# Optimization experiments

Hardware: AMD Instinct MI355X
Metric: run time of the kernel (lower is better)

The kernel has to match this reference:

```python
import jax, jax.numpy as jnp
from jax import lax
import numpy as np

B = 2; Hs = 48; Ws = 48
DIM = 768; NH = 6; NP = 4; DH = DIM // NH; HID = int(DIM * 0.25)
LIN = Hs * Ws                    # feat tokens (single deform level)
LQ = 21 * (Hs * Ws) // 4         # query tokens: (2H*2W)+(H*W)+(H/2*W/2)


def _ln(x, g, b, eps=1e-6):
    m = jnp.mean(x, -1, keepdims=True)
    v = jnp.mean((x - m) ** 2, -1, keepdims=True)
    return (x - m) * lax.rsqrt(v + eps) * g + b


def _bilinear_sample(value, loc, Hf, Wf):
    """value: [B,NH,Hf*Wf,DH]; loc: [B,Lq,NH,NP,2] normalized to [0,1].
    Matches F.grid_sample(align_corners=False, padding_mode='zeros')."""
    Bq, nH = value.shape[0], value.shape[1]
    Lq = loc.shape[1]
    x = loc[..., 0] * Wf - 0.5
    y = loc[..., 1] * Hf - 0.5
    x0 = jnp.floor(x); y0 = jnp.floor(y)
    wx1 = x - x0; wy1 = y - y0
    x0i = x0.astype(jnp.int32); y0i = y0.astype(jnp.int32)

    def tr(a):  # [B,Lq,NH,NP] -> [B,NH,Lq*NP]
        return jnp.transpose(a, (0, 2, 1, 3)).reshape(Bq, nH, Lq * NP)

    def gather(yi, xi):
        valid = ((xi >= 0) & (xi < Wf) & (yi >= 0) & (yi < Hf)).astype(value.dtype)
        idx = jnp.clip(yi, 0, Hf - 1) * Wf + jnp.clip(xi, 0, Wf - 1)
        g = jnp.take_along_axis(value, tr(idx)[..., None], axis=2)  # [B,NH,Lq*NP,DH]
        return g * tr(valid)[..., None]

    out = (gather(y0i, x0i) * tr((1 - wy1) * (1 - wx1))[..., None]
         + gather(y0i, x0i + 1) * tr((1 - wy1) * wx1)[..., None]
         + gather(y0i + 1, x0i) * tr(wy1 * (1 - wx1))[..., None]
         + gather(y0i + 1, x0i + 1) * tr(wy1 * wx1)[..., None])
    return out.reshape(Bq, nH, Lq, NP, DH)


def _dwconv(x_tokens, w, b, h, w_):
    Bq, n_tok, C = x_tokens.shape
    img = jnp.transpose(x_tokens, (0, 2, 1)).reshape(Bq, C, h, w_)
    y = lax.conv_general_dilated(img, w, (1, 1), 'SAME',
                                 dimension_numbers=('NCHW', 'OIHW', 'NCHW'),
                                 feature_group_count=C) + b[None, :, None, None]
    return jnp.transpose(y.reshape(Bq, C, h * w_), (0, 2, 1))


def _forward(query, reference_points, feat, qn_g, qn_b, fn_g, fn_b, vW, vb,
             soW, sob, awW, awb, opW, opb, mn_g, mn_b,
             fc1W, fc1b, dwW, dwb, fc2W, fc2b, H, W):
    Bq, Lq, C = query.shape
    q = _ln(query, qn_g, qn_b)
    v = _ln(feat, fn_g, fn_b) @ vW + vb                             # [B,Lin,C]
    value = jnp.transpose(v.reshape(Bq, -1, NH, DH), (0, 2, 1, 3))  # [B,NH,Lin,DH]
    offs = (q @ soW + sob).reshape(Bq, Lq, NH, NP, 2)
    attw = jax.nn.softmax((q @ awW + awb).reshape(Bq, Lq, NH, NP), axis=-1)
    norm = jnp.asarray([W, H], dtype=q.dtype)                       # (x,y) normalizer
    loc = reference_points.reshape(Bq, Lq, 1, 1, 2) + offs / norm   # [B,Lq,NH,NP,2]
    samp = _bilinear_sample(value, loc, H, W)                       # [B,NH,Lq,NP,DH]
    aw = jnp.transpose(attw, (0, 2, 1, 3))[..., None]               # [B,NH,Lq,NP,1]
    out = jnp.sum(samp * aw, axis=3)                                # [B,NH,Lq,DH]
    out = jnp.transpose(out, (0, 2, 1, 3)).reshape(Bq, Lq, C) @ opW + opb
    x = query + out                                                 # residual
    # multi-scale conv MLP
    h = _ln(x, mn_g, mn_b) @ fc1W + fc1b                            # [B,Lq,HID]
    n = Lq // 21
    h = jnp.concatenate([
        _dwconv(h[:, :16 * n], dwW, dwb, 2 * H, 2 * W),
        _dwconv(h[:, 16 * n:20 * n], dwW, dwb, H, W),
        _dwconv(h[:, 20 * n:], dwW, dwb, H // 2, W // 2)], axis=1)
    h = jax.nn.gelu(h, approximate=False)
    h = h @ fc2W + fc2b
    return x + h


def setup_inputs():
    key = jax.random.key(0)
    ks = jax.random.split(key, 16)
    s = 0.02
    return dict(
        query=jax.random.normal(ks[0], (B, LQ, DIM), jnp.float32),
        reference_points=jax.random.uniform(ks[1], (B, LQ, 1, 2), jnp.float32),
        feat=jax.random.normal(ks[2], (B, LIN, DIM), jnp.float32),
        spatial_shapes=jnp.array([[Hs, Ws]], jnp.int32),
        level_start_index=jnp.array([0], jnp.int32),
        H=Hs, W=Ws,
        qn_g=jnp.ones((DIM,)), qn_b=jnp.zeros((DIM,)),
        fn_g=jnp.ones((DIM,)), fn_b=jnp.zeros((DIM,)),
        mn_g=jnp.ones((DIM,)), mn_b=jnp.zeros((DIM,)),
        vW=s * jax.random.normal(ks[3], (DIM, DIM)), vb=jnp.zeros((DIM,)),
        soW=s * jax.random.normal(ks[4], (DIM, NH * NP * 2)),
        sob=0.5 * jax.random.normal(ks[5], (NH * NP * 2,)),
        awW=s * jax.random.normal(ks[6], (DIM, NH * NP)), awb=jnp.zeros((NH * NP,)),
        opW=s * jax.random.normal(ks[7], (DIM, DIM)), opb=jnp.zeros((DIM,)),
        fc1W=s * jax.random.normal(ks[8], (DIM, HID)), fc1b=jnp.zeros((HID,)),
        dwW=s * jax.random.normal(ks[9], (HID, 1, 3, 3)), dwb=jnp.zeros((HID,)),
        fc2W=s * jax.random.normal(ks[10], (HID, DIM)), fc2b=jnp.zeros((DIM,)),
    )


def reference(query, reference_points, feat, spatial_shapes, level_start_index, H, W,
              qn_g, qn_b, fn_g, fn_b, mn_g, mn_b, vW, vb, soW, sob, awW, awb,
              opW, opb, fc1W, fc1b, dwW, dwb, fc2W, fc2b):
    del spatial_shapes, level_start_index  # single level; H,W are static ints
    return _forward(query, reference_points, feat, qn_g, qn_b, fn_g, fn_b, vW, vb,
                    soW, sob, awW, awb, opW, opb, mn_g, mn_b,
                    fc1W, fc1b, dwW, dwb, fc2W, fc2b, H, W)
```

## Files before the change

kernel.cpp:

```cpp
#include <hip/hip_runtime.h>

#define NB    2
#define LQT   12096
#define LINT  2304
#define DIMC  768
#define NHD   6
#define NPT   4
#define DHD   128
#define HIDC  192
#define HH    48
#define WW    48

typedef __attribute__((ext_vector_type(8))) short bf16x8;
typedef __attribute__((ext_vector_type(4))) float f32x4;

__device__ __forceinline__ unsigned short f2bf(float f) {
  unsigned int u = __builtin_bit_cast(unsigned int, f);
  u += 0x7FFFu + ((u >> 16) & 1u);
  return (unsigned short)(u >> 16);
}
__device__ __forceinline__ float bf2f(unsigned short h) {
  unsigned int u = ((unsigned int)h) << 16;
  return __builtin_bit_cast(float, u);
}

__device__ __forceinline__ void gload16(const unsigned short* g, unsigned short* l) {
  __builtin_amdgcn_global_load_lds(
      (const __attribute__((address_space(1))) unsigned int*)g,
      (__attribute__((address_space(3))) unsigned int*)l, 16, 0, 0);
}

__global__ __launch_bounds__(256) void pack_wt(const float* __restrict__ src,
                                               unsigned short* __restrict__ dst,
                                               int K, int N, int rows) {
  size_t i = (size_t)blockIdx.x * 256 + threadIdx.x;
  if (i >= (size_t)rows * K) return;
  int n = (int)(i / K), k = (int)(i % K);
  float v = (n < N) ? src[(size_t)k * N + n] : 0.f;
  dst[i] = f2bf(v);
}

__global__ __launch_bounds__(256) void pack_soaw(const float* __restrict__ soW,
                                                 const float* __restrict__ awW,
                                                 const float* __restrict__ sob,
                                                 const float* __restrict__ awb,
                                                 unsigned short* __restrict__ dst,
                                                 float* __restrict__ bdst) {
  size_t i = (size_t)blockIdx.x * 256 + threadIdx.x;
  if (i < 128) bdst[i] = (i < 48) ? sob[i] : (i < 72 ? awb[i - 48] : 0.f);
  if (i >= (size_t)128 * DIMC) return;
  int n = (int)(i / DIMC), k = (int)(i % DIMC);
  float v = (n < 48) ? soW[(size_t)k * 48 + n]
                     : (n < 72 ? awW[(size_t)k * 24 + (n - 48)] : 0.f);
  dst[i] = f2bf(v);
}

template <bool IN_BF16>
__global__ __launch_bounds__(256) void ln_to_bf16(const void* __restrict__ in_,
                                                  const float* __restrict__ gamma,
                                                  const float* __restrict__ beta,
                                                  unsigned short* __restrict__ out) {
  const int row = blockIdx.x;
  const int t = threadIdx.x;
  float v0, v1, v2;
  if (IN_BF16) {
    const unsigned short* x = (const unsigned short*)in_ + (size_t)row * DIMC;
    v0 = bf2f(x[t]); v1 = bf2f(x[t + 256]); v2 = bf2f(x[t + 512]);
  } else {
    const float* x = (const float*)in_ + (size_t)row * DIMC;
    v0 = x[t]; v1 = x[t + 256]; v2 = x[t + 512];
  }
  float s = v0 + v1 + v2;
  float s2 = v0 * v0 + v1 * v1 + v2 * v2;
#pragma unroll
  for (int o = 32; o > 0; o >>= 1) {
    s += __shfl_down(s, o);
    s2 += __shfl_down(s2, o);
  }
  __shared__ float red[8];
  const int wave = t >> 6, lane = t & 63;
  if (lane == 0) { red[wave] = s; red[wave + 4] = s2; }
  __syncthreads();
  float S = red[0] + red[1] + red[2] + red[3];
  float S2 = red[4] + red[5] + red[6] + red[7];
  float mean = S * (1.0f / DIMC);
  float var = S2 * (1.0f / DIMC) - mean * mean;
  float inv = rsqrtf(var + 1e-6f);
  unsigned short* o0 = out + (size_t)row * DIMC;
  o0[t]       = f2bf((v0 - mean) * inv * gamma[t]       + beta[t]);
  o0[t + 256] = f2bf((v1 - mean) * inv * gamma[t + 256] + beta[t + 256]);
  o0[t + 512] = f2bf((v2 - mean) * inv * gamma[t + 512] + beta[t + 512]);
}

template <int WM, int WN, bool HAS_ADD, bool ADD_BF16, bool OUT_BF16>
__global__ __launch_bounds__(256) void gemm_bt(const unsigned short* __restrict__ A,
                                               const unsigned short* __restrict__ Bt,
                                               const float* __restrict__ bias,
                                               const void* __restrict__ add_,
                                               void* __restrict__ out_,
                                               int M, int N, int K, int nn) {
  constexpr int BM = 2 * WM * 16;
  constexpr int BN = 2 * WN * 16;
  constexpr int CHA = BM * 8;
  constexpr int CHT = (BM + BN) * 8;
  __shared__ unsigned short As[2][BM * 64];
  __shared__ unsigned short Bs[2][BN * 64];
  const int t = threadIdx.x;
  const int wave = t >> 6, lane = t & 63;

  const int nwg = gridDim.x;
  const int qq = nwg >> 3, rr = nwg & 7;
  const int xcd = blockIdx.x & 7, pos = blockIdx.x >> 3;
  const int swz = ((xcd < rr) ? xcd * (qq + 1) : rr * (qq + 1) + (xcd - rr) * qq) + pos;
  const int m0 = (swz / nn) * BM;
  const int n0 = (swz % nn) * BN;

  const int wm = (wave >> 1) * (WM * 16), wn = (wave & 1) * (WN * 16);
  const int lr = lane & 15;
  const int lg = lane >> 4;

  auto stage = [&](int buf, int k0) {
#pragma unroll
    for (int i = 0; i < CHT / 256; ++i) {
      const int c = t + i * 256;
      if (c < CHA) {
        const int row = c >> 3, slot = c & 7;
        const int ca = slot ^ (row & 7);
        gload16(A + (size_t)(m0 + row) * K + k0 + ca * 8, &As[buf][c * 8]);
      } else {
        const int c2 = c - CHA, row = c2 >> 3, slot = c2 & 7;
        const int ca = slot ^ (row & 7);
        gload16(Bt + (size_t)(n0 + row) * K + k0 + ca * 8, &Bs[buf][c2 * 8]);
      }
    }
  };

  f32x4 acc[WM][WN] = {};

  stage(0, 0);
  __syncthreads();
  int cur = 0;

  for (int k0 = 0; k0 < K; k0 += 64) {
    if (k0 + 64 < K) stage(cur ^ 1, k0 + 64);

    bf16x8 af[2][WM], bg[2][WN];
#pragma unroll
    for (int kk = 0; kk < 2; ++kk) {
#pragma unroll
      for (int i = 0; i < WM; ++i) {
        const int row = wm + i * 16 + lr;
        const int slot = (kk * 4 + lg) ^ (row & 7);
        af[kk][i] = *(const bf16x8*)(&As[cur][row * 64 + slot * 8]);
      }
#pragma unroll
      for (int j = 0; j < WN; ++j) {
        const int row = wn + j * 16 + lr;
        const int slot = (kk * 4 + lg) ^ (row & 7);
        bg[kk][j] = *(const bf16x8*)(&Bs[cur][row * 64 + slot * 8]);
      }
    }
#pragma unroll
    for (int kk = 0; kk < 2; ++kk)
#pragma unroll
      for (int i = 0; i < WM; ++i)
#pragma unroll
        for (int j = 0; j < WN; ++j)
          acc[i][j] = __builtin_amdgcn_mfma_f32_16x16x32_bf16(af[kk][i], bg[kk][j], acc[i][j], 0, 0, 0);

    __syncthreads();
    cur ^= 1;
  }

  const int orow = lg * 4;
  const float* addf = (const float*)add_;
  const unsigned short* addb = (const unsigned short*)add_;
  float* outf = (float*)out_;
  unsigned short* outb = (unsigned short*)out_;
#pragma unroll
  for (int i = 0; i < WM; ++i) {
#pragma unroll
    for (int j = 0; j < WN; ++j) {
      const int n = n0 + wn + j * 16 + lr;
      if (n < N) {
#pragma unroll
        for (int r = 0; r < 4; ++r) {
          const int m = m0 + wm + i * 16 + orow + r;
          if (m < M) {
            float v = acc[i][j][r] + bias[n];
            if (HAS_ADD) v += ADD_BF16 ? bf2f(addb[(size_t)m * N + n]) : addf[(size_t)m * N + n];
            if (OUT_BF16) outb[(size_t)m * N + n] = f2bf(v);
            else          outf[(size_t)m * N + n] = v;
          }
        }
      }
    }
  }
}

#define FCP 42
__global__ __launch_bounds__(512) void fc2_persist(const unsigned short* __restrict__ A,
                                                   const unsigned short* __restrict__ Bt,
                                                   const float* __restrict__ bias,
                                                   const unsigned short* __restrict__ add,
                                                   float* __restrict__ out, int M) {
  __shared__ unsigned short Bp[128 * 192];
  const int t = threadIdx.x;
  const int wave = t >> 6, lane = t & 63;
  const int lr = lane & 15, lg = lane >> 4;
  const int n0 = (blockIdx.x % 6) * 128;
  const int p  = blockIdx.x / 6;
  const int wm = (wave & 3) * 32, wn = (wave >> 2) * 64;

#pragma unroll
  for (int i = 0; i < 6; ++i) {
    const int c = t + i * 512;
    const int row = c / 24, slot = c % 24;
    const int ca = (slot & ~7) | ((slot & 7) ^ (row & 7));
    gload16(Bt + (size_t)(n0 + row) * 192 + ca * 8, &Bp[c * 8]);
  }
  asm volatile("s_waitcnt vmcnt(0)" ::: "memory");
  __syncthreads();

  const int NTILE = M / 128;
  for (int mt = p; mt < NTILE; mt += FCP) {
    const int m0 = mt * 128;
    bf16x8 a[2][6];
#pragma unroll
    for (int u = 0; u < 2; ++u) {
      const unsigned short* ap = A + (size_t)(m0 + wm + u * 16 + lr) * 192 + lg * 8;
#pragma unroll
      for (int ks = 0; ks < 6; ++ks) a[u][ks] = *(const bf16x8*)(ap + ks * 32);
    }
    f32x4 acc[2][4] = {};
#pragma unroll
    for (int ks = 0; ks < 6; ++ks) {
      bf16x8 bg[4];
#pragma unroll
      for (int j = 0; j < 4; ++j) {
        const int row = wn + j * 16 + lr;
        const int sp = ks * 4 + lg;
        const int slot = (sp & ~7) | ((sp & 7) ^ (row & 7));
        bg[j] = *(const bf16x8*)(&Bp[row * 192 + slot * 8]);
      }
#pragma unroll
      for (int u = 0; u < 2; ++u)
#pragma unroll
        for (int j = 0; j < 4; ++j)
          acc[u][j] = __builtin_amdgcn_mfma_f32_16x16x32_bf16(a[u][ks], bg[j], acc[u][j], 0, 0, 0);
    }
#pragma unroll
    for (int u = 0; u < 2; ++u)
#pragma unroll
      for (int j = 0; j < 4; ++j) {
        const int n = n0 + wn + j * 16 + lr;
#pragma unroll
        for (int r = 0; r < 4; ++r) {
          const int m = m0 + wm + u * 16 + lg * 4 + r;
          out[(size_t)m * DIMC + n] = acc[u][j][r] + bias[n] + bf2f(add[(size_t)m * DIMC + n]);
        }
      }
  }
}

__global__ __launch_bounds__(192) void deform_attn(const float* __restrict__ soaw,
                                                   const float* __restrict__ rp,
                                                   const float* __restrict__ value,
                                                   unsigned short* __restrict__ attn) {
  const int row = blockIdx.x;
  const int b = row / LQT;
  const int t = threadIdx.x;
  const int h = t >> 5;
  const int l = t & 31;
  const float* sa = soaw + (size_t)row * 128;
  const float bx = rp[(size_t)row * 2 + 0] * (float)WW - 0.5f;
  const float by = rp[(size_t)row * 2 + 1] * (float)HH - 0.5f;

  float lg0 = sa[48 + h * 4 + 0], lg1 = sa[48 + h * 4 + 1];
  float lg2 = sa[48 + h * 4 + 2], lg3 = sa[48 + h * 4 + 3];
  float mx = fmaxf(fmaxf(lg0, lg1), fmaxf(lg2, lg3));
  float e0 = expf(lg0 - mx), e1 = expf(lg1 - mx), e2 = expf(lg2 - mx), e3 = expf(lg3 - mx);
  float inv = 1.0f / (e0 + e1 + e2 + e3);
  float awp[4] = {e0 * inv, e1 * inv, e2 * inv, e3 * inv};

  const float* vb = value + (size_t)b * LINT * DIMC + h * DHD + l * 4;
  float ax = 0.f, ay = 0.f, az = 0.f, aw = 0.f;
#pragma unroll
  for (int p = 0; p < 4; ++p) {
    float fx = bx + sa[h * 8 + p * 2 + 0];
    float fy = by + sa[h * 8 + p * 2 + 1];
    float x0f = floorf(fx), y0f = floorf(fy);
    float wx = fx - x0f, wy = fy - y0f;
    int x0 = (int)x0f, y0 = (int)y0f;
#pragma unroll
    for (int dy = 0; dy < 2; ++dy) {
#pragma unroll
      for (int dx = 0; dx < 2; ++dx) {
        int xi = x0 + dx, yi = y0 + dy;
        float w = (dy ? wy : 1.f - wy) * (dx ? wx : 1.f - wx) * awp[p];
        if (xi < 0 || xi >= WW || yi < 0 || yi >= HH) w = 0.f;
        int xc = min(max(xi, 0), WW - 1), yc = min(max(yi, 0), HH - 1);
        const float4 g = *(const float4*)(vb + (size_t)(yc * WW + xc) * DIMC);
        ax += w * g.x; ay += w * g.y; az += w * g.z; aw += w * g.w;
      }
    }
  }
  unsigned short* op = attn + (size_t)row * DIMC + h * DHD + l * 4;
  ushort4 ov;
  ov.x = f2bf(ax); ov.y = f2bf(ay); ov.z = f2bf(az); ov.w = f2bf(aw);
  *(ushort4*)op = ov;
}

__global__ __launch_bounds__(192) void dwconv_gelu(const unsigned short* __restrict__ h1,
                                                   const float* __restrict__ dwW,
                                                   const float* __restrict__ dwb,
                                                   unsigned short* __restrict__ out) {
  const int blk = blockIdx.x;
  const int b = blk / LQT;
  const int q = blk % LQT;
  int base, Wi, Hi;
  if (q < 9216)       { base = 0;     Wi = 96; Hi = 96; }
  else if (q < 11520) { base = 9216;  Wi = 48; Hi = 48; }
  else                { base = 11520; Wi = 24; Hi = 24; }
  const int loc = q - base;
  const int y = loc / Wi, x = loc % Wi;
  const int c = threadIdx.x;
  const unsigned short* src = h1 + ((size_t)b * LQT + base) * HIDC + c;
  float acc = dwb[c];
#pragma unroll
  for (int dy = -1; dy <= 1; ++dy) {
    int yy = y + dy;
    if (yy < 0 || yy >= Hi) continue;
#pragma unroll
    for (int dx = -1; dx <= 1; ++dx) {
      int xx = x + dx;
      if (xx < 0 || xx >= Wi) continue;
      acc += dwW[c * 9 + (dy + 1) * 3 + (dx + 1)] * bf2f(src[(size_t)(yy * Wi + xx) * HIDC]);
    }
  }
  float g = 0.5f * acc * (1.0f + erff(acc * 0.70710678118654752f));
  out[(size_t)blk * HIDC + c] = f2bf(g);
}

extern "C" void kernel_launch(void* const* d_in, const int* in_sizes, int n_in,
                              void* d_out, int out_size, void* d_ws, size_t ws_size,
                              hipStream_t stream) {
  const float* query = (const float*)d_in[0];
  const float* rp    = (const float*)d_in[1];
  const float* feat  = (const float*)d_in[2];
  const float* qn_g  = (const float*)d_in[7];
  const float* qn_b  = (const float*)d_in[8];
  const float* fn_g  = (const float*)d_in[9];
  const float* fn_b  = (const float*)d_in[10];
  const float* mn_g  = (const float*)d_in[11];
  const float* mn_b  = (const float*)d_in[12];
  const float* vW    = (const float*)d_in[13];
  const float* vb    = (const float*)d_in[14];
  const float* soW   = (const float*)d_in[15];
  const float* sob   = (const float*)d_in[16];
  const float* awW   = (const float*)d_in[17];
  const float* awb   = (const float*)d_in[18];
  const float* opW   = (const float*)d_in[19];
  const float* opb   = (const float*)d_in[20];
  const float* fc1W  = (const float*)d_in[21];
  const float* fc1b  = (const float*)d_in[22];
  const float* dwW   = (const float*)d_in[23];
  const float* dwb   = (const float*)d_in[24];
  const float* fc2W  = (const float*)d_in[25];
  const float* fc2b  = (const float*)d_in[26];
  float* out = (float*)d_out;
  (void)in_sizes; (void)n_in; (void)out_size; (void)ws_size;

  char* ws = (char*)d_ws;
  size_t off = 0;
  auto alloc = [&](size_t bytes) -> void* {
    off = (off + 255) & ~(size_t)255;
    void* p = ws + off;
    off += bytes;
    return p;
  };

  const int MQ = NB * LQT;
  const int MF = NB * LINT;

  unsigned short* vWt    = (unsigned short*)alloc((size_t)768 * 768 * 2);
  unsigned short* opWt   = (unsigned short*)alloc((size_t)768 * 768 * 2);
  unsigned short* soawWt = (unsigned short*)alloc((size_t)128 * 768 * 2);
  unsigned short* fc1Wt  = (unsigned short*)alloc((size_t)192 * 768 * 2);
  unsigned short* fc2Wt  = (unsigned short*)alloc((size_t)768 * 192 * 2);
  float*          soawb  = (float*)alloc(128 * 4);
  unsigned short* f_ln   = (unsigned short*)alloc((size_t)MF * DIMC * 2);
  unsigned short* q_ln   = (unsigned short*)alloc((size_t)MQ * DIMC * 2);
  float*          value  = (float*)alloc((size_t)MF * DIMC * 4);
  float*          soaw   = (float*)alloc((size_t)MQ * 128 * 4);
  unsigned short* attnb  = (unsigned short*)alloc((size_t)MQ * DIMC * 2);
  unsigned short* xbuf   = (unsigned short*)alloc((size_t)MQ * DIMC * 2);

  unsigned short* h1b = attnb;
  unsigned short* coutb = (unsigned short*)soaw;
  unsigned short* lnx = q_ln;

  pack_wt<<<dim3((768 * 768 + 255) / 256), dim3(256), 0, stream>>>(vW, vWt, 768, 768, 768);
  pack_wt<<<dim3((768 * 768 + 255) / 256), dim3(256), 0, stream>>>(opW, opWt, 768, 768, 768);
  pack_wt<<<dim3((192 * 768 + 255) / 256), dim3(256), 0, stream>>>(fc1W, fc1Wt, 768, 192, 192);
  pack_wt<<<dim3((768 * 192 + 255) / 256), dim3(256), 0, stream>>>(fc2W, fc2Wt, 192, 768, 768);
  pack_soaw<<<dim3((128 * 768 + 255) / 256), dim3(256), 0, stream>>>(soW, awW, sob, awb, soawWt, soawb);

  ln_to_bf16<false><<<dim3(MF), dim3(256), 0, stream>>>(feat, fn_g, fn_b, f_ln);
  ln_to_bf16<false><<<dim3(MQ), dim3(256), 0, stream>>>(query, qn_g, qn_b, q_ln);

  gemm_bt<2, 4, false, false, false><<<dim3((MF / 64) * 6), dim3(256), 0, stream>>>(
      f_ln, vWt, vb, nullptr, value, MF, 768, 768, 6);

  gemm_bt<2, 4, false, false, false><<<dim3(MQ / 64), dim3(256), 0, stream>>>(
      q_ln, soawWt, soawb, nullptr, soaw, MQ, 128, 768, 1);

  deform_attn<<<dim3(MQ), dim3(192), 0, stream>>>(soaw, rp, value, attnb);

  gemm_bt<4, 4, true, false, true><<<dim3((MQ / 128) * 6), dim3(256), 0, stream>>>(
      attnb, opWt, opb, query, xbuf, MQ, 768, 768, 6);

  ln_to_bf16<true><<<dim3(MQ), dim3(256), 0, stream>>>(xbuf, mn_g, mn_b, lnx);

  gemm_bt<4, 2, false, false, true><<<dim3((MQ / 128) * 3), dim3(256), 0, stream>>>(
      lnx, fc1Wt, fc1b, nullptr, h1b, MQ, 192, 768, 3);

  dwconv_gelu<<<dim3(MQ), dim3(192), 0, stream>>>(h1b, dwW, dwb, coutb);

  fc2_persist<<<dim3(6 * FCP), dim3(512), 0, stream>>>(coutb, fc2Wt, fc2b, xbuf, out, MQ);
}
```

Measured before the change: 350.5 us.

## Add 256x256 four-stage pipelined GEMM for out-proj and fc2, keep residual in fp32

Adds a new GEMM kernel with 256x256 tiles, 512 threads, a four-buffer async LDS pipeline and raised wave priority around the MFMAs. It replaces the out-projection GEMM and the persistent fc2 kernel. The intermediate residual buffer moves from bf16 to fp32, which doubles its traffic but removes bf16 rounding. Scratch buffers are padded to 24320 rows so the A tiles can be read past M without checks, while stores stay guarded by m<M. The larger tiles cost more LDS and registers per block, which limits occupancy.

```diff
diff --git a/kernel.cpp b/kernel.cpp
--- a/kernel.cpp
+++ b/kernel.cpp
@@ -55,21 +55,14 @@
   dst[i] = f2bf(v);
 }
 
-template <bool IN_BF16>
-__global__ __launch_bounds__(256) void ln_to_bf16(const void* __restrict__ in_,
+__global__ __launch_bounds__(256) void ln_to_bf16(const float* __restrict__ in,
                                                   const float* __restrict__ gamma,
                                                   const float* __restrict__ beta,
                                                   unsigned short* __restrict__ out) {
   const int row = blockIdx.x;
   const int t = threadIdx.x;
-  float v0, v1, v2;
-  if (IN_BF16) {
-    const unsigned short* x = (const unsigned short*)in_ + (size_t)row * DIMC;
-    v0 = bf2f(x[t]); v1 = bf2f(x[t + 256]); v2 = bf2f(x[t + 512]);
-  } else {
-    const float* x = (const float*)in_ + (size_t)row * DIMC;
-    v0 = x[t]; v1 = x[t + 256]; v2 = x[t + 512];
-  }
+  const float* x = in + (size_t)row * DIMC;
+  float v0 = x[t], v1 = x[t + 256], v2 = x[t + 512];
   float s = v0 + v1 + v2;
   float s2 = v0 * v0 + v1 * v1 + v2 * v2;
 #pragma unroll
@@ -92,11 +85,10 @@
   o0[t + 512] = f2bf((v2 - mean) * inv * gamma[t + 512] + beta[t + 512]);
 }
 
-template <int WM, int WN, bool HAS_ADD, bool ADD_BF16, bool OUT_BF16>
+template <int WM, int WN, bool OUT_BF16>
 __global__ __launch_bounds__(256) void gemm_bt(const unsigned short* __restrict__ A,
                                                const unsigned short* __restrict__ Bt,
                                                const float* __restrict__ bias,
-                                               const void* __restrict__ add_,
                                                void* __restrict__ out_,
                                                int M, int N, int K, int nn) {
   constexpr int BM = 2 * WM * 16;
@@ -173,8 +165,6 @@
   }
 
   const int orow = lg * 4;
-  const float* addf = (const float*)add_;
-  const unsigned short* addb = (const unsigned short*)add_;
   float* outf = (float*)out_;
   unsigned short* outb = (unsigned short*)out_;
 #pragma unroll
@@ -188,7 +178,6 @@
           const int m = m0 + wm + i * 16 + orow + r;
           if (m < M) {
             float v = acc[i][j][r] + bias[n];
-            if (HAS_ADD) v += ADD_BF16 ? bf2f(addb[(size_t)m * N + n]) : addf[(size_t)m * N + n];
             if (OUT_BF16) outb[(size_t)m * N + n] = f2bf(v);
             else          outf[(size_t)m * N + n] = v;
           }
@@ -198,68 +187,96 @@
   }
 }
 
-#define FCP 42
-__global__ __launch_bounds__(512) void fc2_persist(const unsigned short* __restrict__ A,
-                                                   const unsigned short* __restrict__ Bt,
-                                                   const float* __restrict__ bias,
-                                                   const unsigned short* __restrict__ add,
-                                                   float* __restrict__ out, int M) {
-  __shared__ unsigned short Bp[128 * 192];
+__global__ __launch_bounds__(512, 2) void gemm256(const unsigned short* __restrict__ A,
+                                                  const unsigned short* __restrict__ Bt,
+                                                  const float* __restrict__ bias,
+                                                  const float* __restrict__ add,
+                                                  float* __restrict__ out,
+                                                  int M, int N, int K, int nn) {
+  __shared__ unsigned short As[4][256 * 32];
+  __shared__ unsigned short Bs[4][256 * 32];
   const int t = threadIdx.x;
   const int wave = t >> 6, lane = t & 63;
   const int lr = lane & 15, lg = lane >> 4;
-  const int n0 = (blockIdx.x % 6) * 128;
-  const int p  = blockIdx.x / 6;
-  const int wm = (wave & 3) * 32, wn = (wave >> 2) * 64;
-
-#pragma unroll
-  for (int i = 0; i < 6; ++i) {
-    const int c = t + i * 512;
-    const int row = c / 24, slot = c % 24;
-    const int ca = (slot & ~7) | ((slot & 7) ^ (row & 7));
-    gload16(Bt + (size_t)(n0 + row) * 192 + ca * 8, &Bp[c * 8]);
-  }
-  asm volatile("s_waitcnt vmcnt(0)" ::: "memory");
-  __syncthreads();
-
-  const int NTILE = M / 128;
-  for (int mt = p; mt < NTILE; mt += FCP) {
-    const int m0 = mt * 128;
-    bf16x8 a[2][6];
-#pragma unroll
-    for (int u = 0; u < 2; ++u) {
-      const unsigned short* ap = A + (size_t)(m0 + wm + u * 16 + lr) * 192 + lg * 8;
-#pragma unroll
-      for (int ks = 0; ks < 6; ++ks) a[u][ks] = *(const bf16x8*)(ap + ks * 32);
-    }
-    f32x4 acc[2][4] = {};
-#pragma unroll
-    for (int ks = 0; ks < 6; ++ks) {
-      bf16x8 bg[4];
-#pragma unroll
-      for (int j = 0; j < 4; ++j) {
-        const int row = wn + j * 16 + lr;
-        const int sp = ks * 4 + lg;
-        const int slot = (sp & ~7) | ((sp & 7) ^ (row & 7));
-        bg[j] = *(const bf16x8*)(&Bp[row * 192 + slot * 8]);
-      }
-#pragma unroll
-      for (int u = 0; u < 2; ++u)
-#pragma unroll
-        for (int j = 0; j < 4; ++j)
-          acc[u][j] = __builtin_amdgcn_mfma_f32_16x16x32_bf16(a[u][ks], bg[j], acc[u][j], 0, 0, 0);
-    }
-#pragma unroll
-    for (int u = 0; u < 2; ++u)
-#pragma unroll
-      for (int j = 0; j < 4; ++j) {
-        const int n = n0 + wn + j * 16 + lr;
-#pragma unroll
-        for (int r = 0; r < 4; ++r) {
-          const int m = m0 + wm + u * 16 + lg * 4 + r;
-          out[(size_t)m * DIMC + n] = acc[u][j][r] + bias[n] + bf2f(add[(size_t)m * DIMC + n]);
-        }
-      }
+
+  const int nwg = gridDim.x;
+  const int qq = nwg >> 3, rr = nwg & 7;
+  const int xcd = blockIdx.x & 7, pos = blockIdx.x >> 3;
+  const int swz = ((xcd < rr) ? xcd * (qq + 1) : rr * (qq + 1) + (xcd - rr) * qq) + pos;
+  const int m0 = (swz / nn) * 256;
+  const int n0 = (swz % nn) * 256;
+
+  const int wm = (wave >> 2) * 128;
+  const int wn = (wave & 3) * 64;
+
+  auto stage = [&](int buf, int kt) {
+    const int k0 = kt * 32;
+#pragma unroll
+    for (int i = 0; i < 2; ++i) {
+      const int c = t + i * 512;
+      const int row = c >> 2, slot = c & 3;
+      const int ca = slot ^ ((row >> 1) & 3);
+      gload16(A + (size_t)(m0 + row) * K + k0 + ca * 8, &As[buf][c * 8]);
+    }
+#pragma unroll
+    for (int i = 0; i < 2; ++i) {
+      const int c = t + i * 512;
+      const int row = c >> 2, slot = c & 3;
+      const int ca = slot ^ ((row >> 1) & 3);
+      gload16(Bt + (size_t)(n0 + row) * K + k0 + ca * 8, &Bs[buf][c * 8]);
+    }
+  };
+
+  f32x4 acc[8][4] = {};
+  const int NT = K >> 5;
+
+  stage(0, 0);
+  stage(1, 1);
+  stage(2, 2);
+
+  for (int kt = 0; kt < NT; ++kt) {
+    if (kt < NT - 2)       asm volatile("s_waitcnt vmcnt(8)" ::: "memory");
+    else if (kt == NT - 2) asm volatile("s_waitcnt vmcnt(4)" ::: "memory");
+    else                   asm volatile("s_waitcnt vmcnt(0)" ::: "memory");
+    __builtin_amdgcn_s_barrier();
+    asm volatile("" ::: "memory");
+
+    if (kt + 3 < NT) stage((kt + 3) & 3, kt + 3);
+
+    const unsigned short* asb = &As[kt & 3][0];
+    const unsigned short* bsb = &Bs[kt & 3][0];
+    bf16x8 bg[4];
+#pragma unroll
+    for (int j = 0; j < 4; ++j) {
+      const int row = wn + j * 16 + lr;
+      const int slot = lg ^ ((row >> 1) & 3);
+      bg[j] = *(const bf16x8*)(&bsb[row * 32 + slot * 8]);
+    }
+    __builtin_amdgcn_s_setprio(1);
+#pragma unroll
+    for (int mf = 0; mf < 8; ++mf) {
+      const int row = wm + mf * 16 + lr;
+      const int slot = lg ^ ((row >> 1) & 3);
+      const bf16x8 af = *(const bf16x8*)(&asb[row * 32 + slot * 8]);
+#pragma unroll
+      for (int j = 0; j < 4; ++j)
+        acc[mf][j] = __builtin_amdgcn_mfma_f32_16x16x32_bf16(af, bg[j], acc[mf][j], 0, 0, 0);
+    }
+    __builtin_amdgcn_s_setprio(0);
+  }
+
+#pragma unroll
+  for (int mf = 0; mf < 8; ++mf) {
+#pragma unroll
+    for (int j = 0; j < 4; ++j) {
+      const int n = n0 + wn + j * 16 + lr;
+#pragma unroll
+      for (int r = 0; r < 4; ++r) {
+        const int m = m0 + wm + mf * 16 + lg * 4 + r;
+        if (m < M)
+          out[(size_t)m * N + n] = acc[mf][j][r] + bias[n] + add[(size_t)m * N + n];
+      }
+    }
   }
 }
 
@@ -381,6 +398,7 @@
   };
 
   const int MQ = NB * LQT;
+  const int MQP = 24320;
   const int MF = NB * LINT;
 
   unsigned short* vWt    = (unsigned short*)alloc((size_t)768 * 768 * 2);
@@ -392,9 +410,9 @@
   unsigned short* f_ln   = (unsigned short*)alloc((size_t)MF * DIMC * 2);
   unsigned short* q_ln   = (unsigned short*)alloc((size_t)MQ * DIMC * 2);
   float*          value  = (float*)alloc((size_t)MF * DIMC * 4);
-  float*          soaw   = (float*)alloc((size_t)MQ * 128 * 4);
-  unsigned short* attnb  = (unsigned short*)alloc((size_t)MQ * DIMC * 2);
-  unsigned short* xbuf   = (unsigned short*)alloc((size_t)MQ * DIMC * 2);
+  float*          soaw   = (float*)alloc((size_t)MQP * 128 * 4);
+  unsigned short* attnb  = (unsigned short*)alloc((size_t)MQP * DIMC * 2);
+  float*          xbuf   = (float*)alloc((size_t)MQ * DIMC * 4);
 
   unsigned short* h1b = attnb;
   unsigned short* coutb = (unsigned short*)soaw;
@@ -406,26 +424,27 @@
   pack_wt<<<dim3((768 * 192 + 255) / 256), dim3(256), 0, stream>>>(fc2W, fc2Wt, 192, 768, 768);
   pack_soaw<<<dim3((128 * 768 + 255) / 256), dim3(256), 0, stream>>>(soW, awW, sob, awb, soawWt, soawb);
 
-  ln_to_bf16<false><<<dim3(MF), dim3(256), 0, stream>>>(feat, fn_g, fn_b, f_ln);
-  ln_to_bf16<false><<<dim3(MQ), dim3(256), 0, stream>>>(query, qn_g, qn_b, q_ln);
-
-  gemm_bt<2, 4, false, false, false><<<dim3((MF / 64) * 6), dim3(256), 0, stream>>>(
-      f_ln, vWt, vb, nullptr, value, MF, 768, 768, 6);
-
-  gemm_bt<2, 4, false, false, false><<<dim3(MQ / 64), dim3(256), 0, stream>>>(
-      q_ln, soawWt, soawb, nullptr, soaw, MQ, 128, 768, 1);
+  ln_to_bf16<<<dim3(MF), dim3(256), 0, stream>>>(feat, fn_g, fn_b, f_ln);
+  ln_to_bf16<<<dim3(MQ), dim3(256), 0, stream>>>(query, qn_g, qn_b, q_ln);
+
+  gemm_bt<2, 4, false><<<dim3((MF / 64) * 6), dim3(256), 0, stream>>>(
+      f_ln, vWt, vb, value, MF, 768, 768, 6);
+
+  gemm_bt<2, 4, false><<<dim3(MQ / 64), dim3(256), 0, stream>>>(
+      q_ln, soawWt, soawb, soaw, MQ, 128, 768, 1);
 
   deform_attn<<<dim3(MQ), dim3(192), 0, stream>>>(soaw, rp, value, attnb);
 
-  gemm_bt<4, 4, true, false, true><<<dim3((MQ / 128) * 6), dim3(256), 0, stream>>>(
-      attnb, opWt, opb, query, xbuf, MQ, 768, 768, 6);
-
-  ln_to_bf16<true><<<dim3(MQ), dim3(256), 0, stream>>>(xbuf, mn_g, mn_b, lnx);
-
-  gemm_bt<4, 2, false, false, true><<<dim3((MQ / 128) * 3), dim3(256), 0, stream>>>(
-      lnx, fc1Wt, fc1b, nullptr, h1b, MQ, 192, 768, 3);
+  gemm256<<<dim3((MQP / 256) * 3), dim3(512), 0, stream>>>(
+      attnb, opWt, opb, query, xbuf, MQ, 768, 768, 3);
+
+  ln_to_bf16<<<dim3(MQ), dim3(256), 0, stream>>>(xbuf, mn_g, mn_b, lnx);
+
+  gemm_bt<4, 2, true><<<dim3((MQ / 128) * 3), dim3(256), 0, stream>>>(
+      lnx, fc1Wt, fc1b, h1b, MQ, 192, 768, 3);
 
   dwconv_gelu<<<dim3(MQ), dim3(192), 0, stream>>>(h1b, dwW, dwb, coutb);
 
-  fc2_persist<<<dim3(6 * FCP), dim3(512), 0, stream>>>(coutb, fc2Wt, fc2b, xbuf, out, MQ);
-}
+  gemm256<<<dim3((MQP / 256) * 3), dim3(512), 0, stream>>>(
+      coutb, fc2Wt, fc2b, xbuf, out, MQ, 768, 192, 3);
+}
```

New measurement: 461.6 us. +31.7%, slower.
